# Kernel optimization log

Measured on AMD Instinct MI355X. Metric: run time of the kernel, lower is better.

The kernel has to match this reference:

```python
import jax, jax.numpy as jnp
import numpy as np

B, T, C, H = 2, 2048, 1024, 16
N = C // H
MISS_ROWS = 128


def _rwkv7_scan(q, w_log, k, v, a, b):
    # all [B,T,H,N] float32 (bf16-rounded). RWKV7 delta-rule recurrence:
    #   S_t = S_{t-1} * diag(exp(w_t)) + (S_{t-1} a_t) b_t^T + v_t k_t^T
    #   o_t = S_t q_t   (state S has shape [B,H,Nv,Nk]; decay along k-dim)
    Bq, Tq, Hq, Nq = q.shape

    def step(S, inp):
        q_t, w_t, k_t, v_t, a_t, b_t = inp
        ew = jnp.exp(w_t)  # decay in (0,1) since w_log = -exp(...) < 0
        sa = jnp.einsum('bhvi,bhi->bhv', S, a_t)
        S = S * ew[:, :, None, :] + sa[..., None] * b_t[:, :, None, :] + v_t[..., None] * k_t[:, :, None, :]
        o = jnp.einsum('bhvj,bhj->bhv', S, q_t)
        return S, o

    xs = tuple(jnp.moveaxis(u, 1, 0) for u in (q, w_log, k, v, a, b))
    S0 = jnp.zeros((Bq, Hq, Nq, Nq), jnp.float32)
    _, o = jax.lax.scan(step, S0, xs)
    return jnp.moveaxis(o, 0, 1)  # [B,T,H,N]


def setup_inputs() -> dict:
    key = jax.random.key(0)
    ks = jax.random.split(key, 16)
    f32 = jnp.float32
    return {
        'residual': jax.random.normal(ks[0], (B, T, C), f32),
        'x': jax.random.normal(ks[1], (B, T, C), f32),
        'x0': jax.random.normal(ks[2], (B, T, C), f32),
        'dx0': jax.random.normal(ks[3], (B, T, C), f32),
        'Wq': jax.random.normal(ks[4], (C, C), f32) * 0.02,
        'Wk': jax.random.normal(ks[5], (C, C), f32) * 0.02,
        'Wv': jax.random.normal(ks[6], (C, C), f32) * 0.02,
        'Wproj': jax.random.normal(ks[7], (C, C), f32) * 0.02,
        'x_q': jax.random.uniform(ks[8], (1, 1, C), f32),
        'x_k': jax.random.uniform(ks[9], (1, 1, C), f32),
        'x_v': jax.random.uniform(ks[10], (1, 1, C), f32),
        'v0': 0.7 + 0.1 * jax.random.normal(ks[11], (1, 1, C), f32),
        'w0': -3.0 + 0.5 * jax.random.normal(ks[12], (1, 1, C), f32),
        'a0': 0.1 * jax.random.normal(ks[13], (1, 1, C), f32),
        'miss': jax.random.normal(ks[14], (MISS_ROWS, 4 * C), f32) * 0.02,
        'r_k': 0.1 * jax.random.normal(ks[15], (H, N), f32),
    }


def reference(residual, x, x0, dx0, Wq, Wk, Wv, Wproj, x_q, x_k, x_v, v0, w0, a0, miss, r_k):
    Bx, Tx, Cx = x.shape
    Hh, Nn = r_k.shape
    # token shift: dx_prev = x_{t-1} - x_t (zero-padded at t=0)
    dx_prev = jnp.concatenate([jnp.zeros_like(x[:, :1]), x[:, :-1]], axis=1) - x
    q = (x + dx_prev * x_q) @ Wq.T
    k = (x + dx_prev * x_k) @ Wk.T
    v = (x + dx_prev * x_v) @ Wv.T
    deltas = x[:, :, :miss.shape[0]] @ miss  # [B,T,4C]
    w_delta, v_delta, a_delta, g = jnp.split(deltas, 4, axis=-1)
    log_neglog_w = -jax.nn.softplus(-(w0 + w_delta)) - 0.5
    log_w = -jnp.exp(log_neglog_w)  # log decay, always < 0
    v_first = (x0 + dx0 * x_v) @ Wv.T
    v = v + (v_first - v) * jax.nn.sigmoid(v0 + v_delta)
    g = 1.0 + g
    a = jax.nn.sigmoid(a0 + a_delta)
    kh = k.reshape(Bx, Tx, Hh, Nn)
    kk = kh / jnp.maximum(jnp.linalg.norm(kh, axis=-1, keepdims=True), 1e-12)
    kk = kk.reshape(Bx, Tx, Cx)
    k = k * a
    z = -kk
    b = kk * a
    bf = lambda u: u.astype(jnp.bfloat16).astype(jnp.float32).reshape(Bx, Tx, Hh, Nn)
    qh, wh, kh2, vh, zh, bh = (bf(u) for u in (q, log_w, k, v, z, b))
    y = _rwkv7_scan(qh, wh, kh2, vh, zh, bh) * (float(Nn) ** -0.5)  # [B,T,H,N]
    xnorm = jnp.linalg.norm(x.reshape(Bx, Tx, Hh, Nn), axis=-1, keepdims=True)
    vnorm = jnp.linalg.norm(vh, axis=-1, keepdims=True)
    u = (1.0 - xnorm / (vnorm + 1e-12)) * jax.nn.sigmoid(r_k)
    y = (y + vh * u).reshape(Bx, Tx, Cx)
    y = y * g
    return residual + y @ Wproj.T
```

## Files before the change

kernel.cpp:

```cpp
#include <hip/hip_runtime.h>
#include <stdint.h>
#include <stddef.h>

#define B_ 2
#define T_ 2048
#define C_ 1024
#define H_ 16
#define N_ 64
#define M_ (B_*T_)
#define L_ 128
#define NC_ (T_/L_)

typedef unsigned short ushort_t;
typedef __attribute__((ext_vector_type(8))) __bf16 bf16x8;
typedef __attribute__((ext_vector_type(4))) float  f32x4;

__device__ __forceinline__ ushort_t f2bf(float x){
  uint32_t u = __float_as_uint(x);
  u += 0x7fffu + ((u >> 16) & 1u);
  return (ushort_t)(u >> 16);
}
__device__ __forceinline__ float bf2f(uint32_t hu){
  return __uint_as_float(hu << 16);
}
__device__ __forceinline__ float quad_sum(float v){
  float a = __int_as_float(__builtin_amdgcn_mov_dpp(__float_as_int(v), 0xB1, 0xF, 0xF, true));
  v += a;
  float b = __int_as_float(__builtin_amdgcn_mov_dpp(__float_as_int(v), 0x4E, 0xF, 0xF, true));
  return v + b;
}

__device__ __forceinline__ ushort4 mixq4(float4 a, float4 p, float4 c){
  ushort4 o;
  o.x = f2bf(fmaf(p.x - a.x, c.x, a.x));
  o.y = f2bf(fmaf(p.y - a.y, c.y, a.y));
  o.z = f2bf(fmaf(p.z - a.z, c.z, a.z));
  o.w = f2bf(fmaf(p.w - a.w, c.w, a.w));
  return o;
}
__global__ __launch_bounds__(256) void prep_all(
    const float* __restrict__ x, const float* __restrict__ x0,
    const float* __restrict__ dx0,
    const float* __restrict__ xq, const float* __restrict__ xk,
    const float* __restrict__ xv,
    const float* __restrict__ Wq, const float* __restrict__ Wk,
    const float* __restrict__ Wv, const float* __restrict__ Wp,
    const float* __restrict__ miss,
    ushort_t* __restrict__ Aq, ushort_t* __restrict__ Ak,
    ushort_t* __restrict__ Av, ushort_t* __restrict__ Axf,
    ushort_t* __restrict__ Xb,
    ushort_t* __restrict__ Wb, ushort_t* __restrict__ Wpb,
    ushort_t* __restrict__ missT)
{
  __shared__ ushort_t tile[128][66];
  const int blk = blockIdx.x;
  const int tid = threadIdx.x;
  if (blk < 4096){
    const int idx = blk*256 + tid;
    const int col4 = idx & 255;
    const int i = idx >> 8;
    const int t = i & (T_-1);
    float4 a = ((const float4*)x)[idx];
    float4 p = {0.f,0.f,0.f,0.f};
    if (t > 0) p = ((const float4*)x)[idx - 256];
    float4 cq = ((const float4*)xq)[col4];
    float4 ck = ((const float4*)xk)[col4];
    float4 cv = ((const float4*)xv)[col4];
    ((ushort4*)Aq)[idx] = mixq4(a, p, cq);
    ((ushort4*)Ak)[idx] = mixq4(a, p, ck);
    ((ushort4*)Av)[idx] = mixq4(a, p, cv);
    float4 z = ((const float4*)x0)[idx];
    float4 d = ((const float4*)dx0)[idx];
    ushort4 of;
    of.x = f2bf(fmaf(d.x, cv.x, z.x));
    of.y = f2bf(fmaf(d.y, cv.y, z.y));
    of.z = f2bf(fmaf(d.z, cv.z, z.z));
    of.w = f2bf(fmaf(d.w, cv.w, z.w));
    ((ushort4*)Axf)[idx] = of;
    ushort4 ob = {f2bf(a.x), f2bf(a.y), f2bf(a.z), f2bf(a.w)};
    ((ushort4*)Xb)[idx] = ob;
  } else if (blk < 4096 + 5*1024){
    const int y = (blk - 4096) >> 10;
    const float* src = (y==0)?Wq:(y==1)?Wk:(y<4)?Wv:Wp;
    ushort_t* dst = (y<4) ? Wb + (size_t)y*C_*C_ : Wpb;
    const int idx = ((blk - 4096) & 1023)*256 + tid;
    float4 v = ((const float4*)src)[idx];
    ushort4 o = {f2bf(v.x), f2bf(v.y), f2bf(v.z), f2bf(v.w)};
    ((ushort4*)dst)[idx] = o;
  } else {
    const int j0 = (blk - 4096 - 5*1024)*64;
#pragma unroll
    for (int rep=0; rep<8; rep++){
      int k = rep*16 + (tid>>4);
      int jj = (tid&15)*4;
      float4 v = *(const float4*)&miss[(size_t)k*4096 + j0 + jj];
      tile[k][jj+0]=f2bf(v.x); tile[k][jj+1]=f2bf(v.y);
      tile[k][jj+2]=f2bf(v.z); tile[k][jj+3]=f2bf(v.w);
    }
    __syncthreads();
#pragma unroll
    for (int rep=0; rep<8; rep++){
      int j = tid>>2;
      int kk = (tid&3)*32 + rep*4;
      ushort4 o = {tile[kk+0][j], tile[kk+1][j], tile[kk+2][j], tile[kk+3][j]};
      *(ushort4*)&missT[(size_t)(j0+j)*128 + kk] = o;
    }
  }
}

__global__ __launch_bounds__(256, 2) void mfma_gemm(
    const ushort_t* __restrict__ Ab, int lda, int64_t Asz,
    const ushort_t* __restrict__ Bbp, int ldb, int64_t Bsz,
    void* __restrict__ Cb, int ldc, int64_t Csz, int c_bf16,
    const float* __restrict__ resid, int K)
{
  const ushort_t* A  = Ab  + (size_t)blockIdx.z * Asz;
  const ushort_t* Bm = Bbp + (size_t)blockIdx.z * Bsz;
  const int i0 = blockIdx.y * 128;
  const int j0 = blockIdx.x * 128;
  const int tid = threadIdx.x;
  const int lane = tid & 63;
  const int w = tid >> 6;
  const int wm = w & 1, wn = w >> 1;

  __shared__ ushort_t As[128*32];
  __shared__ ushort_t Bs[128*32];

  f32x4 acc[4][4];
#pragma unroll
  for (int i=0;i<4;i++)
#pragma unroll
    for (int j=0;j<4;j++) acc[i][j] = (f32x4){0.f,0.f,0.f,0.f};

  const int lr = lane >> 2;
  const int ls = lane & 3;
  const ushort_t* ga = A  + (size_t)(i0 + w*32 + lr)*lda + ls*8;
  const ushort_t* gb = Bm + (size_t)(j0 + w*32 + lr)*ldb + ls*8;
  const int lm = lane & 15, lq = lane >> 4;

  for (int k0 = 0; k0 < K; k0 += 32){
    __syncthreads();
#pragma unroll
    for (int p=0;p<2;p++){
      __builtin_amdgcn_global_load_lds(
        (const __attribute__((address_space(1))) void*)(ga + (size_t)p*16*lda + k0),
        (__attribute__((address_space(3))) void*)&As[(w*32 + p*16)*32], 16, 0, 0);
      __builtin_amdgcn_global_load_lds(
        (const __attribute__((address_space(1))) void*)(gb + (size_t)p*16*ldb + k0),
        (__attribute__((address_space(3))) void*)&Bs[(w*32 + p*16)*32], 16, 0, 0);
    }
    __syncthreads();
    bf16x8 af[4], bfr[4];
#pragma unroll
    for (int i=0;i<4;i++)
      af[i] = *(const bf16x8*)&As[(wm*64 + i*16 + lm)*32 + lq*8];
#pragma unroll
    for (int j=0;j<4;j++)
      bfr[j] = *(const bf16x8*)&Bs[(wn*64 + j*16 + lm)*32 + lq*8];
#pragma unroll
    for (int i=0;i<4;i++)
#pragma unroll
      for (int j=0;j<4;j++)
        acc[i][j] = __builtin_amdgcn_mfma_f32_16x16x32_bf16(af[i], bfr[j], acc[i][j], 0, 0, 0);
  }

  if (!c_bf16){
    float* C = (float*)Cb + (size_t)blockIdx.z * Csz;
#pragma unroll
    for (int i=0;i<4;i++)
#pragma unroll
      for (int j=0;j<4;j++)
#pragma unroll
        for (int r=0;r<4;r++){
          const int row = i0 + wm*64 + i*16 + lq*4 + r;
          const int col = j0 + wn*64 + j*16 + lm;
          float v = acc[i][j][r];
          if (resid) v += resid[(size_t)row*ldc + col];
          C[(size_t)row*ldc + col] = v;
        }
  } else {
    ushort_t* C = (ushort_t*)Cb + (size_t)blockIdx.z * Csz;
#pragma unroll
    for (int i=0;i<4;i++)
#pragma unroll
      for (int j=0;j<4;j++)
#pragma unroll
        for (int r=0;r<4;r++){
          const int row = i0 + wm*64 + i*16 + lq*4 + r;
          const int col = j0 + wn*64 + j*16 + lm;
          C[(size_t)row*ldc + col] = f2bf(acc[i][j][r]);
        }
  }
}

__global__ __launch_bounds__(256, 2) void qkvm_gemm(
    const ushort_t* __restrict__ Ab4, const ushort_t* __restrict__ Wb,
    const ushort_t* __restrict__ Xb,  const ushort_t* __restrict__ missT,
    float* __restrict__ qkvf, ushort_t* __restrict__ delb)
{
  const int bid = blockIdx.x;
  const bool isQKV = bid < 1024;
  const ushort_t* A; const ushort_t* Bm;
  int i0, j0, ldb, K, z = 0;
  if (isQKV){
    z = bid >> 8;
    const int g = bid & 255;
    j0 = (g & 7) * 128;
    i0 = (g >> 3) * 128;
    A  = Ab4 + (size_t)z*M_*C_;
    Bm = Wb  + (size_t)z*C_*C_;
    ldb = C_; K = C_;
  } else {
    const int g = bid - 1024;
    j0 = (g & 31) * 128;
    i0 = (g >> 5) * 128;
    A = Xb; Bm = missT;
    ldb = 128; K = 128;
  }
  const int lda = C_;
  const int tid = threadIdx.x;
  const int lane = tid & 63;
  const int w = tid >> 6;
  const int wm = w & 1, wn = w >> 1;

  __shared__ ushort_t As[128*32];
  __shared__ ushort_t Bs[128*32];

  f32x4 acc[4][4];
#pragma unroll
  for (int i=0;i<4;i++)
#pragma unroll
    for (int j=0;j<4;j++) acc[i][j] = (f32x4){0.f,0.f,0.f,0.f};

  const int lr = lane >> 2;
  const int ls = lane & 3;
  const ushort_t* ga = A  + (size_t)(i0 + w*32 + lr)*lda + ls*8;
  const ushort_t* gb = Bm + (size_t)(j0 + w*32 + lr)*ldb + ls*8;
  const int lm = lane & 15, lq = lane >> 4;

  for (int k0 = 0; k0 < K; k0 += 32){
    __syncthreads();
#pragma unroll
    for (int p=0;p<2;p++){
      __builtin_amdgcn_global_load_lds(
        (const __attribute__((address_space(1))) void*)(ga + (size_t)p*16*lda + k0),
        (__attribute__((address_space(3))) void*)&As[(w*32 + p*16)*32], 16, 0, 0);
      __builtin_amdgcn_global_load_lds(
        (const __attribute__((address_space(1))) void*)(gb + (size_t)p*16*ldb + k0),
        (__attribute__((address_space(3))) void*)&Bs[(w*32 + p*16)*32], 16, 0, 0);
    }
    __syncthreads();
    bf16x8 af[4], bfr[4];
#pragma unroll
    for (int i=0;i<4;i++)
      af[i] = *(const bf16x8*)&As[(wm*64 + i*16 + lm)*32 + lq*8];
#pragma unroll
    for (int j=0;j<4;j++)
      bfr[j] = *(const bf16x8*)&Bs[(wn*64 + j*16 + lm)*32 + lq*8];
#pragma unroll
    for (int i=0;i<4;i++)
#pragma unroll
      for (int j=0;j<4;j++)
        acc[i][j] = __builtin_amdgcn_mfma_f32_16x16x32_bf16(af[i], bfr[j], acc[i][j], 0, 0, 0);
  }

  if (isQKV){
    float* C = qkvf + (size_t)z*M_*C_;
#pragma unroll
    for (int i=0;i<4;i++)
#pragma unroll
      for (int j=0;j<4;j++)
#pragma unroll
        for (int r=0;r<4;r++){
          const int row = i0 + wm*64 + i*16 + lq*4 + r;
          const int col = j0 + wn*64 + j*16 + lm;
          C[(size_t)row*C_ + col] = acc[i][j][r];
        }
  } else {
#pragma unroll
    for (int i=0;i<4;i++)
#pragma unroll
      for (int j=0;j<4;j++)
#pragma unroll
        for (int r=0;r<4;r++){
          const int row = i0 + wm*64 + i*16 + lq*4 + r;
          const int col = j0 + wn*64 + j*16 + lm;
          delb[(size_t)row*(4*C_) + col] = f2bf(acc[i][j][r]);
        }
  }
}

__global__ __launch_bounds__(256) void fuse_kernel(
    const float* __restrict__ qm, const float* __restrict__ km,
    const float* __restrict__ vm, const float* __restrict__ vfm,
    const ushort_t* __restrict__ del, const float* __restrict__ x,
    const float* __restrict__ w0, const float* __restrict__ v0,
    const float* __restrict__ a0,
    uint32_t* __restrict__ packed, float* __restrict__ gout,
    float* __restrict__ ratio)
{
  const int lane = threadIdx.x & 63;
  const int ht = blockIdx.x*4 + (threadIdx.x >> 6);
  const int i = ht >> 4;
  const int h = ht & 15;
  const int c = h*64 + lane;
  const size_t ic = (size_t)i*C_ + c;
  float qv = qm[ic], kv = km[ic], vv = vm[ic], vfv = vfm[ic], xv = x[ic];
  const size_t d0 = (size_t)i*4*C_ + c;
  float wd = bf2f(del[d0]), vd = bf2f(del[d0+C_]);
  float ad = bf2f(del[d0+2*C_]), gd = bf2f(del[d0+3*C_]);

  float z1 = -(w0[c]+wd);
  float sp = fmaxf(z1, 0.f) + log1pf(expf(-fabsf(z1)));
  float logw = -expf(-sp - 0.5f);
  float sv = 1.f/(1.f+expf(-(v0[c]+vd)));
  vv = vv + (vfv - vv)*sv;
  float gv = 1.f + gd;
  float av = 1.f/(1.f+expf(-(a0[c]+ad)));

  ushort_t vr_u = f2bf(vv);
  float vrf = bf2f(vr_u);

  float ksq = kv*kv, xsq = xv*xv, vsq = vrf*vrf;
#pragma unroll
  for (int off=32; off>0; off>>=1){
    ksq += __shfl_xor(ksq, off, 64);
    xsq += __shfl_xor(xsq, off, 64);
    vsq += __shfl_xor(vsq, off, 64);
  }
  float kn = sqrtf(ksq);
  float kkn = kv / fmaxf(kn, 1e-12f);
  float k2 = kv*av;
  float zv = -kkn;
  float bv = kkn*av;

  uint32_t p0 = (uint32_t)f2bf(logw) | ((uint32_t)f2bf(zv) << 16);
  uint32_t p1 = (uint32_t)f2bf(bv)   | ((uint32_t)f2bf(k2) << 16);
  uint32_t p2 = (uint32_t)f2bf(qv)   | ((uint32_t)vr_u << 16);
  uint32_t* pb = packed + ((size_t)ht*64 + lane)*3;
  pb[0]=p0; pb[1]=p1; pb[2]=p2;
  gout[ic] = gv;
  if (lane == 0)
    ratio[ht] = 1.f - sqrtf(xsq)/(sqrtf(vsq)+1e-12f);
}


__global__ __launch_bounds__(512, 4) void chunk_mdp_kernel(
    const uint32_t* __restrict__ packed,
    float* __restrict__ phi, float* __restrict__ cc, float* __restrict__ md)
{
  const int tid  = threadIdx.x;
  const int role = tid >> 8;
  const int row  = (tid >> 2) & 63;
  const int qr   = tid & 3;

  __shared__ float ewS[8][N_], zS[8][N_], bS[8][N_], kS[8][N_], qS[8][N_], vS[8][N_];

  const int g  = blockIdx.x;
  const int cx = g & (NC_-1), bh = g >> 4;
  const int b = bh >> 4, h = bh & 15;
  const size_t pbase = ((size_t)(b*T_ + cx*L_)*H_ + h)*64;

  const int ls = tid >> 6;
  const int ld = tid & 63;

  uint32_t pu0, pu1, pu2;
  {
    size_t ap = (pbase + (size_t)ls*(H_*64) + ld)*3;
    pu0 = packed[ap]; pu1 = packed[ap+1]; pu2 = packed[ap+2];
  }

  float R[16];
  if (role == 0){
#pragma unroll
    for (int i=0;i<16;i++) R[i] = (qr*16+i == row) ? 1.f : 0.f;
  } else {
#pragma unroll
    for (int i=0;i<16;i++) R[i] = 0.f;
  }

  for (int tg = 0; tg < L_; tg += 8){
    __syncthreads();
    ewS[ls][ld] = __expf(bf2f(pu0 & 0xffffu));
    zS[ls][ld]  = bf2f(pu0 >> 16);
    bS[ls][ld]  = bf2f(pu1 & 0xffffu);
    kS[ls][ld]  = bf2f(pu1 >> 16);
    qS[ls][ld]  = bf2f(pu2 & 0xffffu);
    vS[ls][ld]  = bf2f(pu2 >> 16);
    if (tg + 8 < L_){
      size_t ap = (pbase + (size_t)(tg+8+ls)*(H_*64) + ld)*3;
      pu0 = packed[ap]; pu1 = packed[ap+1]; pu2 = packed[ap+2];
    }
    __syncthreads();
#pragma unroll 1
    for (int ss=0; ss<8; ss++){
      const float* zr = &zS[ss][qr*16];
      float s_ = 0.f;
#pragma unroll
      for (int i4=0;i4<4;i4++){
        float4 z4 = *(const float4*)&zr[i4*4];
        s_ = fmaf(R[i4*4+0], z4.x, s_);
        s_ = fmaf(R[i4*4+1], z4.y, s_);
        s_ = fmaf(R[i4*4+2], z4.z, s_);
        s_ = fmaf(R[i4*4+3], z4.w, s_);
      }
      s_ = quad_sum(s_);
      const float* er = &ewS[ss][qr*16];
      const float* br = &bS[ss][qr*16];
      const float* qrp = &qS[ss][qr*16];
      float o = 0.f;
      if (role == 0){
#pragma unroll
        for (int i4=0;i4<4;i4++){
          float4 e4 = *(const float4*)&er[i4*4];
          float4 b4 = *(const float4*)&br[i4*4];
          float4 q4 = *(const float4*)&qrp[i4*4];
          float t;
          t = fmaf(R[i4*4+0], e4.x, s_*b4.x); R[i4*4+0]=t; o = fmaf(t, q4.x, o);
          t = fmaf(R[i4*4+1], e4.y, s_*b4.y); R[i4*4+1]=t; o = fmaf(t, q4.y, o);
          t = fmaf(R[i4*4+2], e4.z, s_*b4.z); R[i4*4+2]=t; o = fmaf(t, q4.z, o);
          t = fmaf(R[i4*4+3], e4.w, s_*b4.w); R[i4*4+3]=t; o = fmaf(t, q4.w, o);
        }
      } else {
        const float* kr = &kS[ss][qr*16];
        const float vr = vS[ss][row];
#pragma unroll
        for (int i4=0;i4<4;i4++){
          float4 e4 = *(const float4*)&er[i4*4];
          float4 b4 = *(const float4*)&br[i4*4];
          float4 q4 = *(const float4*)&qrp[i4*4];
          float4 k4 = *(const float4*)&kr[i4*4];
          float t;
          t = fmaf(R[i4*4+0], e4.x, fmaf(s_, b4.x, vr*k4.x)); R[i4*4+0]=t; o = fmaf(t, q4.x, o);
          t = fmaf(R[i4*4+1], e4.y, fmaf(s_, b4.y, vr*k4.y)); R[i4*4+1]=t; o = fmaf(t, q4.y, o);
          t = fmaf(R[i4*4+2], e4.z, fmaf(s_, b4.z, vr*k4.z)); R[i4*4+2]=t; o = fmaf(t, q4.z, o);
          t = fmaf(R[i4*4+3], e4.w, fmaf(s_, b4.w, vr*k4.w)); R[i4*4+3]=t; o = fmaf(t, q4.w, o);
        }
      }
      o = quad_sum(o);
      if (qr == 0)
        md[((size_t)g*L_ + tg+ss)*128 + role*64 + row] = o;
    }
  }
  float* dst = (role == 0) ? phi : cc;
  const size_t base = (size_t)g*4096 + (size_t)row*64 + qr*16;
#pragma unroll
  for (int i4=0;i4<4;i4++)
    *(float4*)&dst[base + i4*4] = (float4){R[i4*4+0],R[i4*4+1],R[i4*4+2],R[i4*4+3]};
}

__global__ __launch_bounds__(256) void chunk_state_kernel(
    const float* __restrict__ phi, const float* __restrict__ cc,
    float* __restrict__ sstart)
{
  const int mq = blockIdx.x;
  const int bh = blockIdx.y;
  const int tid = threadIdx.x;
  const int rb = tid >> 4;
  const int cq = tid & 15;
  const int row = mq*16 + rb;
  __shared__ float Sld[16][65];
  __shared__ float Fld[64][68];
  float acc[4] = {0.f, 0.f, 0.f, 0.f};
  *(float4*)&Sld[rb][cq*4] = (float4){0.f,0.f,0.f,0.f};
  const float* pc = phi + (size_t)bh*NC_*4096;
  const float* cb = cc  + (size_t)bh*NC_*4096;
  float4 pf[4], pcc;
#pragma unroll
  for (int p=0;p<4;p++) pf[p] = *(const float4*)&pc[(size_t)p*1024 + tid*4];
  pcc = *(const float4*)&cb[(size_t)row*64 + cq*4];

  for (int c=0;c<NC_;c++){
    __syncthreads();
#pragma unroll
    for (int p=0;p<4;p++){
      int f = p*1024 + tid*4;
      *(float4*)&Fld[f>>6][f&63] = pf[p];
    }
    float na[4] = {pcc.x, pcc.y, pcc.z, pcc.w};
    *(float4*)&sstart[(size_t)(bh*NC_+c)*4096 + (size_t)row*64 + cq*4] =
        (float4){acc[0],acc[1],acc[2],acc[3]};
    if (c+1 < NC_){
#pragma unroll
      for (int p=0;p<4;p++) pf[p] = *(const float4*)&pc[(size_t)(c+1)*4096 + p*1024 + tid*4];
      pcc = *(const float4*)&cb[(size_t)(c+1)*4096 + (size_t)row*64 + cq*4];
    }
    __syncthreads();
#pragma unroll 1
    for (int k0=0;k0<64;k0+=4){
      const float4 sr = *(const float4*)&Sld[rb][k0];
      const float4 f0 = *(const float4*)&Fld[k0+0][cq*4];
      const float4 f1 = *(const float4*)&Fld[k0+1][cq*4];
      const float4 f2 = *(const float4*)&Fld[k0+2][cq*4];
      const float4 f3 = *(const float4*)&Fld[k0+3][cq*4];
      na[0] = fmaf(sr.x, f0.x, na[0]); na[0] = fmaf(sr.y, f1.x, na[0]);
      na[0] = fmaf(sr.z, f2.x, na[0]); na[0] = fmaf(sr.w, f3.x, na[0]);
      na[1] = fmaf(sr.x, f0.y, na[1]); na[1] = fmaf(sr.y, f1.y, na[1]);
      na[1] = fmaf(sr.z, f2.y, na[1]); na[1] = fmaf(sr.w, f3.y, na[1]);
      na[2] = fmaf(sr.x, f0.z, na[2]); na[2] = fmaf(sr.y, f1.z, na[2]);
      na[2] = fmaf(sr.z, f2.z, na[2]); na[2] = fmaf(sr.w, f3.z, na[2]);
      na[3] = fmaf(sr.x, f0.w, na[3]); na[3] = fmaf(sr.y, f1.w, na[3]);
      na[3] = fmaf(sr.z, f2.w, na[3]); na[3] = fmaf(sr.w, f3.w, na[3]);
    }
    __syncthreads();
    *(float4*)&Sld[rb][cq*4] = (float4){na[0],na[1],na[2],na[3]};
#pragma unroll
    for (int i=0;i<4;i++) acc[i] = na[i];
  }
}

__global__ __launch_bounds__(256) void chunk_emit_kernel(
    const uint32_t* __restrict__ packed, const float* __restrict__ ratio,
    const float* __restrict__ g, const float* __restrict__ rk,
    const float* __restrict__ sstart, const float* __restrict__ md,
    ushort_t* __restrict__ y)
{
  const int blk = blockIdx.x;
  const int c  = blk & (NC_-1);
  const int bh = blk >> 4;
  const int b = bh >> 4, h = bh & 15;
  const int tid = threadIdx.x;
  const int v = tid & 63;
  const int tg = tid >> 6;

  float4 sr[16];
  const float4* sp = (const float4*)(sstart + (size_t)blk*4096 + (size_t)v*64);
#pragma unroll
  for (int f=0;f<16;f++) sr[f] = sp[f];
  const float sigrk = 1.f/(1.f+__expf(-rk[h*64+v]));

#pragma unroll 1
  for (int ss=0; ss<32; ss++){
    const int t = tg*32 + ss;
    const int token = b*T_ + c*L_ + t;
    const float* mrow = md + ((size_t)blk*L_ + t)*128;
    float o0=0.f,o1=0.f,o2=0.f,o3=0.f;
#pragma unroll
    for (int f=0;f<16;f+=4){
      float4 m0 = ((const float4*)mrow)[f+0];
      float4 m1 = ((const float4*)mrow)[f+1];
      float4 m2 = ((const float4*)mrow)[f+2];
      float4 m3 = ((const float4*)mrow)[f+3];
      o0 = fmaf(sr[f+0].x,m0.x, fmaf(sr[f+0].y,m0.y, fmaf(sr[f+0].z,m0.z, fmaf(sr[f+0].w,m0.w, o0))));
      o1 = fmaf(sr[f+1].x,m1.x, fmaf(sr[f+1].y,m1.y, fmaf(sr[f+1].z,m1.z, fmaf(sr[f+1].w,m1.w, o1))));
      o2 = fmaf(sr[f+2].x,m2.x, fmaf(sr[f+2].y,m2.y, fmaf(sr[f+2].z,m2.z, fmaf(sr[f+2].w,m2.w, o2))));
      o3 = fmaf(sr[f+3].x,m3.x, fmaf(sr[f+3].y,m3.y, fmaf(sr[f+3].z,m3.z, fmaf(sr[f+3].w,m3.w, o3))));
    }
    float o = ((o0+o1)+(o2+o3)) + mrow[64 + v];
    const float vt = bf2f(packed[(((size_t)token*H_ + h)*64 + v)*3 + 2] >> 16);
    const float uv = ratio[(size_t)token*H_ + h];
    const float gv = g[(size_t)token*C_ + h*64 + v];
    y[(size_t)token*C_ + h*64 + v] = f2bf((o*0.125f + vt*uv*sigrk)*gv);
  }
}

extern "C" void kernel_launch(void* const* d_in, const int* in_sizes, int n_in,
                              void* d_out, int out_size, void* d_ws, size_t ws_size,
                              hipStream_t stream)
{
  const float* residual = (const float*)d_in[0];
  const float* x    = (const float*)d_in[1];
  const float* x0   = (const float*)d_in[2];
  const float* dx0  = (const float*)d_in[3];
  const float* Wq   = (const float*)d_in[4];
  const float* Wk   = (const float*)d_in[5];
  const float* Wv   = (const float*)d_in[6];
  const float* Wpr  = (const float*)d_in[7];
  const float* x_q  = (const float*)d_in[8];
  const float* x_k  = (const float*)d_in[9];
  const float* x_v  = (const float*)d_in[10];
  const float* v0   = (const float*)d_in[11];
  const float* w0   = (const float*)d_in[12];
  const float* a0   = (const float*)d_in[13];
  const float* miss = (const float*)d_in[14];
  const float* rk   = (const float*)d_in[15];
  float* out = (float*)d_out;

  char* ws = (char*)d_ws;
  const size_t MB = (size_t)1 << 20;
  float*    q_m    = (float*)(ws + 0*MB);
  float*    k_m    = (float*)(ws + 16*MB);
  float*    v_m    = (float*)(ws + 32*MB);
  float*    vf_m   = (float*)(ws + 48*MB);
  ushort_t* delb   = (ushort_t*)(ws + 64*MB);
  ushort_t* Ab     = (ushort_t*)(ws + 96*MB);
  ushort_t* Xb     = (ushort_t*)(ws + 128*MB);
  ushort_t* Wb     = (ushort_t*)(ws + 136*MB);
  uint32_t* packed = (uint32_t*)(ws + 96*MB);
  float*    g_m    = (float*)(ws + 144*MB);
  ushort_t* Wpb    = (ushort_t*)(ws + 160*MB);
  ushort_t* missT  = (ushort_t*)(ws + 162*MB);
  float*    ratio  = (float*)(ws + 163*MB);
  float*    phi    = (float*)(ws + 0*MB);
  float*    cc     = (float*)(ws + 16*MB);
  float*    sstart = (float*)(ws + 32*MB);
  ushort_t* yb     = (ushort_t*)(ws + 48*MB);
  float*    mdbuf  = (float*)(ws + 64*MB);

  ushort_t* Aq  = Ab + 0*(size_t)M_*C_;
  ushort_t* Ak  = Ab + 1*(size_t)M_*C_;
  ushort_t* Av  = Ab + 2*(size_t)M_*C_;
  ushort_t* Axf = Ab + 3*(size_t)M_*C_;

  dim3 blk(256);
  prep_all<<<4096 + 5*1024 + 64, blk, 0, stream>>>(
      x, x0, dx0, x_q, x_k, x_v, Wq, Wk, Wv, Wpr, miss,
      Aq, Ak, Av, Axf, Xb, Wb, Wpb, missT);
  qkvm_gemm<<<2048, blk, 0, stream>>>(Ab, Wb, Xb, missT, q_m, delb);
  fuse_kernel<<<M_*H_/4, blk, 0, stream>>>(q_m, k_m, v_m, vf_m, delb, x, w0, v0, a0, packed, g_m, ratio);
  chunk_mdp_kernel<<<B_*H_*NC_, dim3(512), 0, stream>>>(packed, phi, cc, mdbuf);
  chunk_state_kernel<<<dim3(4, B_*H_), blk, 0, stream>>>(phi, cc, sstart);
  chunk_emit_kernel<<<B_*H_*NC_, blk, 0, stream>>>(packed, ratio, g_m, rk, sstart, mdbuf, yb);
  mfma_gemm<<<dim3(C_/128, M_/128, 1), blk, 0, stream>>>(
      yb, C_, 0, Wpb, C_, 0, out, C_, 0, 0, residual, C_);
}
```

Measured before the change: 475.3 us.

## Fuse elementwise preprocessing into chunk_mdp kernel and drop packed intermediate

Removes the separate fuse_kernel. The chunk_mdp kernel now reads q/k/v/vfirst/x and the bf16 deltas directly and computes decay, normalised k, a-gating and the v mix inline while staging into shared memory. It writes only the bf16 v and the per-head ratio for the emit kernel, and the emit kernel recomputes g from the delta buffer. This saves one launch and the round trips of the packed and g buffers. In exchange it adds transcendental work and more global loads to the latency-sensitive sequential chunk kernel, which has only 512 blocks. The workspace layout is reshuffled to avoid aliasing.

```diff
diff --git a/kernel.cpp b/kernel.cpp
--- a/kernel.cpp
+++ b/kernel.cpp
@@ -290,64 +290,15 @@
   }
 }
 
-__global__ __launch_bounds__(256) void fuse_kernel(
+
+__global__ __launch_bounds__(512, 4) void chunk_mdp_kernel(
     const float* __restrict__ qm, const float* __restrict__ km,
     const float* __restrict__ vm, const float* __restrict__ vfm,
-    const ushort_t* __restrict__ del, const float* __restrict__ x,
+    const float* __restrict__ x, const ushort_t* __restrict__ delb,
     const float* __restrict__ w0, const float* __restrict__ v0,
     const float* __restrict__ a0,
-    uint32_t* __restrict__ packed, float* __restrict__ gout,
-    float* __restrict__ ratio)
-{
-  const int lane = threadIdx.x & 63;
-  const int ht = blockIdx.x*4 + (threadIdx.x >> 6);
-  const int i = ht >> 4;
-  const int h = ht & 15;
-  const int c = h*64 + lane;
-  const size_t ic = (size_t)i*C_ + c;
-  float qv = qm[ic], kv = km[ic], vv = vm[ic], vfv = vfm[ic], xv = x[ic];
-  const size_t d0 = (size_t)i*4*C_ + c;
-  float wd = bf2f(del[d0]), vd = bf2f(del[d0+C_]);
-  float ad = bf2f(del[d0+2*C_]), gd = bf2f(del[d0+3*C_]);
-
-  float z1 = -(w0[c]+wd);
-  float sp = fmaxf(z1, 0.f) + log1pf(expf(-fabsf(z1)));
-  float logw = -expf(-sp - 0.5f);
-  float sv = 1.f/(1.f+expf(-(v0[c]+vd)));
-  vv = vv + (vfv - vv)*sv;
-  float gv = 1.f + gd;
-  float av = 1.f/(1.f+expf(-(a0[c]+ad)));
-
-  ushort_t vr_u = f2bf(vv);
-  float vrf = bf2f(vr_u);
-
-  float ksq = kv*kv, xsq = xv*xv, vsq = vrf*vrf;
-#pragma unroll
-  for (int off=32; off>0; off>>=1){
-    ksq += __shfl_xor(ksq, off, 64);
-    xsq += __shfl_xor(xsq, off, 64);
-    vsq += __shfl_xor(vsq, off, 64);
-  }
-  float kn = sqrtf(ksq);
-  float kkn = kv / fmaxf(kn, 1e-12f);
-  float k2 = kv*av;
-  float zv = -kkn;
-  float bv = kkn*av;
-
-  uint32_t p0 = (uint32_t)f2bf(logw) | ((uint32_t)f2bf(zv) << 16);
-  uint32_t p1 = (uint32_t)f2bf(bv)   | ((uint32_t)f2bf(k2) << 16);
-  uint32_t p2 = (uint32_t)f2bf(qv)   | ((uint32_t)vr_u << 16);
-  uint32_t* pb = packed + ((size_t)ht*64 + lane)*3;
-  pb[0]=p0; pb[1]=p1; pb[2]=p2;
-  gout[ic] = gv;
-  if (lane == 0)
-    ratio[ht] = 1.f - sqrtf(xsq)/(sqrtf(vsq)+1e-12f);
-}
-
-
-__global__ __launch_bounds__(512, 4) void chunk_mdp_kernel(
-    const uint32_t* __restrict__ packed,
-    float* __restrict__ phi, float* __restrict__ cc, float* __restrict__ md)
+    float* __restrict__ phi, float* __restrict__ cc, float* __restrict__ md,
+    ushort_t* __restrict__ vb, float* __restrict__ ratio)
 {
   const int tid  = threadIdx.x;
   const int role = tid >> 8;
@@ -359,15 +310,20 @@
   const int g  = blockIdx.x;
   const int cx = g & (NC_-1), bh = g >> 4;
   const int b = bh >> 4, h = bh & 15;
-  const size_t pbase = ((size_t)(b*T_ + cx*L_)*H_ + h)*64;
+  const int t0 = b*T_ + cx*L_;
 
   const int ls = tid >> 6;
   const int ld = tid & 63;
-
-  uint32_t pu0, pu1, pu2;
+  const int cdim = h*64 + ld;
+  const float w0c = w0[cdim], v0c = v0[cdim], a0c = a0[cdim];
+
+  float pq, pk, pv, pvf, px;
+  ushort_t dwd, dvd, dad;
   {
-    size_t ap = (pbase + (size_t)ls*(H_*64) + ld)*3;
-    pu0 = packed[ap]; pu1 = packed[ap+1]; pu2 = packed[ap+2];
+    size_t ic = (size_t)(t0 + ls)*C_ + cdim;
+    pq = qm[ic]; pk = km[ic]; pv = vm[ic]; pvf = vfm[ic]; px = x[ic];
+    size_t d0 = (size_t)(t0 + ls)*4*C_ + cdim;
+    dwd = delb[d0]; dvd = delb[d0+C_]; dad = delb[d0+2*C_];
   }
 
   float R[16];
@@ -381,15 +337,41 @@
 
   for (int tg = 0; tg < L_; tg += 8){
     __syncthreads();
-    ewS[ls][ld] = __expf(bf2f(pu0 & 0xffffu));
-    zS[ls][ld]  = bf2f(pu0 >> 16);
-    bS[ls][ld]  = bf2f(pu1 & 0xffffu);
-    kS[ls][ld]  = bf2f(pu1 >> 16);
-    qS[ls][ld]  = bf2f(pu2 & 0xffffu);
-    vS[ls][ld]  = bf2f(pu2 >> 16);
+    {
+      float wd = bf2f(dwd), vd = bf2f(dvd), ad = bf2f(dad);
+      float z1 = -(w0c + wd);
+      float sp = fmaxf(z1, 0.f) + log1pf(expf(-fabsf(z1)));
+      float logw = -expf(-sp - 0.5f);
+      float sv = 1.f/(1.f+expf(-(v0c + vd)));
+      float vvm = pv + (pvf - pv)*sv;
+      float av = 1.f/(1.f+expf(-(a0c + ad)));
+      ushort_t vr_u = f2bf(vvm);
+      float vrf = bf2f(vr_u);
+      float ksq = pk*pk, xsq = px*px, vsq = vrf*vrf;
+#pragma unroll
+      for (int off=32; off>0; off>>=1){
+        ksq += __shfl_xor(ksq, off, 64);
+        xsq += __shfl_xor(xsq, off, 64);
+        vsq += __shfl_xor(vsq, off, 64);
+      }
+      float kn = sqrtf(ksq);
+      float kkn = pk / fmaxf(kn, 1e-12f);
+      ewS[ls][ld] = __expf(bf2f(f2bf(logw)));
+      zS[ls][ld]  = bf2f(f2bf(-kkn));
+      bS[ls][ld]  = bf2f(f2bf(kkn*av));
+      kS[ls][ld]  = bf2f(f2bf(pk*av));
+      qS[ls][ld]  = bf2f(f2bf(pq));
+      vS[ls][ld]  = vrf;
+      const int tok = t0 + tg + ls;
+      vb[(size_t)tok*C_ + cdim] = vr_u;
+      if (ld == 0)
+        ratio[(size_t)tok*H_ + h] = 1.f - sqrtf(xsq)/(sqrtf(vsq)+1e-12f);
+    }
     if (tg + 8 < L_){
-      size_t ap = (pbase + (size_t)(tg+8+ls)*(H_*64) + ld)*3;
-      pu0 = packed[ap]; pu1 = packed[ap+1]; pu2 = packed[ap+2];
+      size_t ic = (size_t)(t0 + tg+8+ls)*C_ + cdim;
+      pq = qm[ic]; pk = km[ic]; pv = vm[ic]; pvf = vfm[ic]; px = x[ic];
+      size_t d0 = (size_t)(t0 + tg+8+ls)*4*C_ + cdim;
+      dwd = delb[d0]; dvd = delb[d0+C_]; dad = delb[d0+2*C_];
     }
     __syncthreads();
 #pragma unroll 1
@@ -510,8 +492,8 @@
 }
 
 __global__ __launch_bounds__(256) void chunk_emit_kernel(
-    const uint32_t* __restrict__ packed, const float* __restrict__ ratio,
-    const float* __restrict__ g, const float* __restrict__ rk,
+    const ushort_t* __restrict__ vb, const ushort_t* __restrict__ delb,
+    const float* __restrict__ ratio, const float* __restrict__ rk,
     const float* __restrict__ sstart, const float* __restrict__ md,
     ushort_t* __restrict__ y)
 {
@@ -547,9 +529,9 @@
       o3 = fmaf(sr[f+3].x,m3.x, fmaf(sr[f+3].y,m3.y, fmaf(sr[f+3].z,m3.z, fmaf(sr[f+3].w,m3.w, o3))));
     }
     float o = ((o0+o1)+(o2+o3)) + mrow[64 + v];
-    const float vt = bf2f(packed[(((size_t)token*H_ + h)*64 + v)*3 + 2] >> 16);
+    const float vt = bf2f(vb[(size_t)token*C_ + h*64 + v]);
     const float uv = ratio[(size_t)token*H_ + h];
-    const float gv = g[(size_t)token*C_ + h*64 + v];
+    const float gv = 1.f + bf2f(delb[(size_t)token*4*C_ + 3*C_ + h*64 + v]);
     y[(size_t)token*C_ + h*64 + v] = f2bf((o*0.125f + vt*uv*sigrk)*gv);
   }
 }
@@ -586,16 +568,15 @@
   ushort_t* Ab     = (ushort_t*)(ws + 96*MB);
   ushort_t* Xb     = (ushort_t*)(ws + 128*MB);
   ushort_t* Wb     = (ushort_t*)(ws + 136*MB);
-  uint32_t* packed = (uint32_t*)(ws + 96*MB);
-  float*    g_m    = (float*)(ws + 144*MB);
   ushort_t* Wpb    = (ushort_t*)(ws + 160*MB);
   ushort_t* missT  = (ushort_t*)(ws + 162*MB);
   float*    ratio  = (float*)(ws + 163*MB);
-  float*    phi    = (float*)(ws + 0*MB);
-  float*    cc     = (float*)(ws + 16*MB);
-  float*    sstart = (float*)(ws + 32*MB);
+  float*    mdbuf  = (float*)(ws + 96*MB);
+  float*    phi    = (float*)(ws + 128*MB);
+  float*    cc     = (float*)(ws + 136*MB);
+  float*    sstart = (float*)(ws + 144*MB);
+  ushort_t* vb     = (ushort_t*)(ws + 152*MB);
   ushort_t* yb     = (ushort_t*)(ws + 48*MB);
-  float*    mdbuf  = (float*)(ws + 64*MB);
 
   ushort_t* Aq  = Ab + 0*(size_t)M_*C_;
   ushort_t* Ak  = Ab + 1*(size_t)M_*C_;
@@ -607,10 +588,10 @@
       x, x0, dx0, x_q, x_k, x_v, Wq, Wk, Wv, Wpr, miss,
       Aq, Ak, Av, Axf, Xb, Wb, Wpb, missT);
   qkvm_gemm<<<2048, blk, 0, stream>>>(Ab, Wb, Xb, missT, q_m, delb);
-  fuse_kernel<<<M_*H_/4, blk, 0, stream>>>(q_m, k_m, v_m, vf_m, delb, x, w0, v0, a0, packed, g_m, ratio);
-  chunk_mdp_kernel<<<B_*H_*NC_, dim3(512), 0, stream>>>(packed, phi, cc, mdbuf);
+  chunk_mdp_kernel<<<B_*H_*NC_, dim3(512), 0, stream>>>(
+      q_m, k_m, v_m, vf_m, x, delb, w0, v0, a0, phi, cc, mdbuf, vb, ratio);
   chunk_state_kernel<<<dim3(4, B_*H_), blk, 0, stream>>>(phi, cc, sstart);
-  chunk_emit_kernel<<<B_*H_*NC_, blk, 0, stream>>>(packed, ratio, g_m, rk, sstart, mdbuf, yb);
+  chunk_emit_kernel<<<B_*H_*NC_, blk, 0, stream>>>(vb, delb, ratio, rk, sstart, mdbuf, yb);
   mfma_gemm<<<dim3(C_/128, M_/128, 1), blk, 0, stream>>>(
       yb, C_, 0, Wpb, C_, 0, out, C_, 0, 0, residual, C_);
 }
```

After: 473.0 us. No clear change (-0.5%).
